# Performance work log

Hardware: AMD Instinct MI355X
Metric: run time of the kernel (lower is better)

The kernel has to match this reference:

```python
import jax, jax.numpy as jnp
import numpy as np

NUM_HEADS = 16


def setup_inputs() -> dict:
    key = jax.random.key(0)
    ks = jax.random.split(key, 6)
    B, N, M, C = 2, 2048, 2048, 1024
    return {
        "reference_data": jax.random.normal(ks[0], (B, N, C), dtype=jnp.float32),
        "target_data": jax.random.normal(ks[1], (B, M, C), dtype=jnp.float32),
        "Wq": jax.random.normal(ks[2], (C, C), dtype=jnp.float32) * (C ** -0.5),
        "Wkv": jax.random.normal(ks[3], (C, 2 * C), dtype=jnp.float32) * (C ** -0.5),
        "Wproj": jax.random.normal(ks[4], (C, C), dtype=jnp.float32) * (C ** -0.5),
        "bproj": jnp.zeros((C,), dtype=jnp.float32),
    }


def reference(reference_data, target_data, Wq, Wkv, Wproj, bproj):
    B, N, C = reference_data.shape
    M = target_data.shape[1]
    H = NUM_HEADS
    hd = C // H
    scale = hd ** -0.5
    # k, v from reference: [B, N, 2, H, hd] -> two [B, H, N, hd]
    kv = (reference_data @ Wkv).reshape(B, N, 2, H, hd)
    k = jnp.transpose(kv[:, :, 0], (0, 2, 1, 3))  # [B,H,N,hd]
    v = jnp.transpose(kv[:, :, 1], (0, 2, 1, 3))  # [B,H,N,hd]
    # q from target: [B, H, M, hd]
    q = jnp.transpose((target_data @ Wq).reshape(B, M, H, hd), (0, 2, 1, 3))
    attn = jnp.einsum("bhid,bhjd->bhij", q, k) * scale  # [B,H,M,N]
    attn = jax.nn.softmax(attn, axis=-1)
    x = jnp.einsum("bhij,bhjd->bhid", attn, v)  # [B,H,M,hd]
    x = jnp.transpose(x, (0, 2, 1, 3)).reshape(B, M, C)
    return x @ Wproj + bproj
```

## Files before the change

kernel.cpp:

```cpp
#include <hip/hip_runtime.h>
#include <hip/hip_bf16.h>
#include <stdint.h>

#define SEQ   2048
#define CH    1024
#define NH    16
#define HD    64

typedef short bf8 __attribute__((ext_vector_type(8)));
typedef short bf4 __attribute__((ext_vector_type(4)));
typedef float f4  __attribute__((ext_vector_type(4)));
typedef unsigned short u16;

#define GAS(p) ((const __attribute__((address_space(1))) void*)(p))
#define LAS(p) ((__attribute__((address_space(3))) void*)(p))

__device__ __forceinline__ u16 f2bf(float f) {
  uint32_t u = __float_as_uint(f);
  u += 0x7fffu + ((u >> 16) & 1u);
  return (u16)(u >> 16);
}

__device__ __forceinline__ uint32_t pk2bf(float a, float b) {
  float2 f; f.x = a; f.y = b;
  __hip_bfloat162 h = __float22bfloat162_rn(f);
  union { __hip_bfloat162 h; uint32_t u; } cv; cv.h = h;
  return cv.u;
}

__device__ __forceinline__ f4 MFMA32(bf8 a, bf8 b, f4 c) {
  return __builtin_amdgcn_mfma_f32_16x16x32_bf16(a, b, c, 0, 0, 0);
}

__device__ __forceinline__ f4 MFMA16(bf4 a, bf4 b, f4 c) {
#if __has_builtin(__builtin_amdgcn_mfma_f32_16x16x16_bf16)
  return __builtin_amdgcn_mfma_f32_16x16x16_bf16(a, b, c, 0, 0, 0);
#elif __has_builtin(__builtin_amdgcn_mfma_f32_16x16x16bf16_1k)
  return __builtin_amdgcn_mfma_f32_16x16x16bf16_1k(a, b, c, 0, 0, 0);
#else
  f4 d = c;
  asm volatile("v_mfma_f32_16x16x16_bf16 %0, %1, %2, %0"
               : "+v"(d) : "v"(a), "v"(b));
  return d;
#endif
}

__global__ void prep(const float* __restrict__ ref, u16* __restrict__ refb,
                     const float* __restrict__ tgt, u16* __restrict__ tgtb,
                     const float* __restrict__ Wq, u16* __restrict__ Wqt,
                     const float* __restrict__ Wkv, u16* __restrict__ Wkvt,
                     const float* __restrict__ Wp, u16* __restrict__ Wpt) {
  __shared__ float tile[32][33];
  int blk = blockIdx.x;
  int t = threadIdx.x;
  if (blk < 8192) {
    const float* in; u16* out;
    if (blk < 4096) { in = ref; out = refb; } else { in = tgt; out = tgtb; blk -= 4096; }
    int i = (blk * 256 + t) * 4;
    float4 f = *reinterpret_cast<const float4*>(in + i);
    ushort4 o;
    o.x = f2bf(f.x); o.y = f2bf(f.y); o.z = f2bf(f.z); o.w = f2bf(f.w);
    *reinterpret_cast<ushort4*>(out + i) = o;
    return;
  }
  blk -= 8192;
  int x = blk & 127, by = blk >> 7;
  const float* in; u16* out; int N;
  if (x < 32)       { in = Wq;  out = Wqt;  N = CH;     }
  else if (x < 96)  { in = Wkv; out = Wkvt; N = 2 * CH; x -= 32; }
  else              { in = Wp;  out = Wpt;  N = CH;     x -= 96; }
  const int K = CH;
  int bn = x * 32, bk = by * 32;
  int tx = t & 31, ty = t >> 5;
  #pragma unroll
  for (int i = ty; i < 32; i += 8)
    tile[i][tx] = in[(size_t)(bk + i) * N + bn + tx];
  __syncthreads();
  #pragma unroll
  for (int i = ty; i < 32; i += 8)
    out[(size_t)(bn + i) * K + bk + tx] = f2bf(tile[tx][i]);
}

__global__ __launch_bounds__(256, 3)
void gemm_qkv(const u16* __restrict__ tgtb, const u16* __restrict__ refb,
              const u16* __restrict__ Wqt, const u16* __restrict__ Wkvt,
              u16* __restrict__ qb, u16* __restrict__ karr, u16* __restrict__ varr)
{
  __shared__ __align__(16) u16 As[2][4096];
  __shared__ __align__(16) u16 Bs[2][4096];
  const int tid = threadIdx.x;
  const int lane = tid & 63, wave = tid >> 6;
  const int l16 = lane & 15, q = lane >> 4;
  const bool isQ = blockIdx.x >= 16;
  const u16* A  = isQ ? tgtb : refb;
  const u16* Bt = isQ ? Wqt : Wkvt;
  const int n0 = (isQ ? (blockIdx.x - 16) : blockIdx.x) * 128;
  const int m0 = blockIdx.y * 128;
  const int wm = (wave >> 1) * 64, wn = (wave & 1) * 64;
  const int Kdim = CH;
  const int c = tid, c2 = tid + 256;
  const int ar = c >> 2, ac = (c & 3) << 3, ar2 = c2 >> 2, ac2 = (c2 & 3) << 3;

  f4 acc[4][4] = {};

  #define STAGE_G(buf, k0)                                                      \
    { __builtin_amdgcn_global_load_lds(                                         \
          GAS(&A[(size_t)(m0 + ar) * Kdim + (k0) + ac]),                        \
          LAS(&As[buf][c << 3]), 16, 0, 0);                                     \
      __builtin_amdgcn_global_load_lds(                                         \
          GAS(&A[(size_t)(m0 + ar2) * Kdim + (k0) + ac2]),                      \
          LAS(&As[buf][c2 << 3]), 16, 0, 0);                                    \
      __builtin_amdgcn_global_load_lds(                                         \
          GAS(&Bt[(size_t)(n0 + ar) * Kdim + (k0) + ac]),                       \
          LAS(&Bs[buf][c << 3]), 16, 0, 0);                                     \
      __builtin_amdgcn_global_load_lds(                                         \
          GAS(&Bt[(size_t)(n0 + ar2) * Kdim + (k0) + ac2]),                     \
          LAS(&Bs[buf][c2 << 3]), 16, 0, 0); }

  STAGE_G(0, 0);
  for (int kk = 0; kk < 32; ++kk) {
    __syncthreads();
    if (kk < 31) STAGE_G((kk + 1) & 1, (kk + 1) * 32);
    const u16* as = As[kk & 1];
    const u16* bs = Bs[kk & 1];
    bf8 a[4], b[4];
    #pragma unroll
    for (int i = 0; i < 4; ++i)
      a[i] = *reinterpret_cast<const bf8*>(&as[(wm + i * 16 + l16) * 32 + q * 8]);
    #pragma unroll
    for (int j = 0; j < 4; ++j)
      b[j] = *reinterpret_cast<const bf8*>(&bs[(wn + j * 16 + l16) * 32 + q * 8]);
    #pragma unroll
    for (int i = 0; i < 4; ++i)
      #pragma unroll
      for (int j = 0; j < 4; ++j)
        acc[i][j] = MFMA32(a[i], b[j], acc[i][j]);
  }
  #undef STAGE_G

  #pragma unroll
  for (int i = 0; i < 4; ++i) {
    const int mbase = m0 + wm + i * 16 + q * 4;
    const int b = mbase >> 11, ns0 = mbase & (SEQ - 1);
    #pragma unroll
    for (int j = 0; j < 4; ++j) {
      const int n = n0 + wn + j * 16 + l16;
      if (isQ) {
        int h = n >> 6, d = n & 63;
        #pragma unroll
        for (int r = 0; r < 4; ++r)
          qb[(size_t)((b * NH + h) * SEQ + ns0 + r) * HD + d] =
              f2bf(acc[i][j][r] * 0.1803368801f);
      } else if (n < CH) {
        int h = n >> 6, d = n & 63;
        size_t base = (size_t)(b * NH + h) * SEQ * HD;
        int off = (((ns0 >> 4) * 2 + (d >> 5)) * 4 + ((d >> 3) & 3)) * 128
                  + (d & 7);
        #pragma unroll
        for (int r = 0; r < 4; ++r)
          karr[base + off + ((ns0 + r) & 15) * 8] = f2bf(acc[i][j][r]);
      } else {
        int c2v = n - CH, h = c2v >> 6, d = c2v & 63;
        size_t base = (size_t)(b * NH + h) * SEQ * HD;
        int off = (((ns0 >> 4) * 2 + (d >> 5)) * 4 + ((ns0 >> 2) & 3)) * 128
                  + (d & 15) * 8 + ((d >> 4) & 1) * 4;
        ushort4 st;
        st.x = f2bf(acc[i][j][0]); st.y = f2bf(acc[i][j][1]);
        st.z = f2bf(acc[i][j][2]); st.w = f2bf(acc[i][j][3]);
        *reinterpret_cast<ushort4*>(&varr[base + off]) = st;
      }
    }
  }
}

__global__ __launch_bounds__(256, 2)
void gemm_proj(const u16* __restrict__ A, const u16* __restrict__ Bt,
               float* __restrict__ fo, const float* __restrict__ bias)
{
  __shared__ __align__(16) u16 As[2][2048];
  __shared__ __align__(16) u16 Bs[2][4096];
  const int tid = threadIdx.x;
  const int lane = tid & 63, wave = tid >> 6;
  const int l16 = lane & 15, q = lane >> 4;
  const int m0 = blockIdx.y * 64, n0 = blockIdx.x * 128;
  const int wm = (wave >> 1) * 32, wn = (wave & 1) * 64;
  const int Kdim = CH;
  const int c = tid, c2 = tid + 256;
  const int ar = c >> 2, ac = (c & 3) << 3, ar2 = c2 >> 2, ac2 = (c2 & 3) << 3;

  f4 acc[2][4] = {};

  #define STAGE_P(buf, k0)                                                      \
    { __builtin_amdgcn_global_load_lds(                                         \
          GAS(&A[(size_t)(m0 + (ar >> 1)) * Kdim + (k0) + ((c & 7) << 2) * 2]), \
          LAS(&As[buf][(c & 255) << 3]), 16, 0, 0);                             \
      __builtin_amdgcn_global_load_lds(                                         \
          GAS(&Bt[(size_t)(n0 + ar) * Kdim + (k0) + ac]),                       \
          LAS(&Bs[buf][c << 3]), 16, 0, 0);                                     \
      __builtin_amdgcn_global_load_lds(                                         \
          GAS(&Bt[(size_t)(n0 + ar2) * Kdim + (k0) + ac2]),                     \
          LAS(&Bs[buf][c2 << 3]), 16, 0, 0); }

  #undef STAGE_P
  const int aar = c >> 2;
  const int aac = (c & 3) << 3;
  #define STAGE_P(buf, k0)                                                      \
    { __builtin_amdgcn_global_load_lds(                                         \
          GAS(&A[(size_t)(m0 + aar) * Kdim + (k0) + aac]),                      \
          LAS(&As[buf][c << 3]), 16, 0, 0);                                     \
      __builtin_amdgcn_global_load_lds(                                         \
          GAS(&Bt[(size_t)(n0 + ar) * Kdim + (k0) + ac]),                       \
          LAS(&Bs[buf][c << 3]), 16, 0, 0);                                     \
      __builtin_amdgcn_global_load_lds(                                         \
          GAS(&Bt[(size_t)(n0 + ar2) * Kdim + (k0) + ac2]),                     \
          LAS(&Bs[buf][c2 << 3]), 16, 0, 0); }

  STAGE_P(0, 0);
  for (int kk = 0; kk < 32; ++kk) {
    __syncthreads();
    if (kk < 31) STAGE_P((kk + 1) & 1, (kk + 1) * 32);
    const u16* as = As[kk & 1];
    const u16* bs = Bs[kk & 1];
    bf8 a[2], b[4];
    #pragma unroll
    for (int i = 0; i < 2; ++i)
      a[i] = *reinterpret_cast<const bf8*>(&as[(wm + i * 16 + l16) * 32 + q * 8]);
    #pragma unroll
    for (int j = 0; j < 4; ++j)
      b[j] = *reinterpret_cast<const bf8*>(&bs[(wn + j * 16 + l16) * 32 + q * 8]);
    #pragma unroll
    for (int i = 0; i < 2; ++i)
      #pragma unroll
      for (int j = 0; j < 4; ++j)
        acc[i][j] = MFMA32(a[i], b[j], acc[i][j]);
  }
  #undef STAGE_P

  #pragma unroll
  for (int i = 0; i < 2; ++i) {
    const int mbase = m0 + wm + i * 16 + q * 4;
    #pragma unroll
    for (int j = 0; j < 4; ++j) {
      const int n = n0 + wn + j * 16 + l16;
      #pragma unroll
      for (int r = 0; r < 4; ++r)
        fo[(size_t)(mbase + r) * CH + n] = acc[i][j][r] + bias[n];
    }
  }
}

__global__ __launch_bounds__(512, 4)
void attn(const u16* __restrict__ Q, const u16* __restrict__ Karr,
          const u16* __restrict__ Varr, u16* __restrict__ X)
{
  __shared__ __align__(16) u16 Ks[2][8192];
  __shared__ __align__(16) u16 Vs[2][8192];
  const int tid = threadIdx.x;
  const int lane = tid & 63;
  const int l16 = lane & 15, q = lane >> 4;
  const int bh = blockIdx.y;
  const int m0 = blockIdx.x * 128;
  const int wm = (tid >> 6) * 16;

  const u16* Qb = Q    + (size_t)bh * SEQ * HD;
  const u16* Kb = Karr + (size_t)bh * SEQ * HD;
  const u16* Vb = Varr + (size_t)bh * SEQ * HD;

  bf8 qf[2];
  #pragma unroll
  for (int ks = 0; ks < 2; ++ks)
    qf[ks] = *reinterpret_cast<const bf8*>(
        &Qb[(size_t)(m0 + wm + l16) * HD + ks * 32 + q * 8]);

  const short one_bf = 0x3F80;
  const bf4 ones = {one_bf, one_bf, one_bf, one_bf};

  f4 o[4] = {};
  f4 ds = {};

  #define STAGE_A(buf, t)                                                       \
    { const u16* kg = Kb + (size_t)(t) * 8192;                                  \
      const u16* vg = Vb + (size_t)(t) * 8192;                                  \
      _Pragma("unroll")                                                         \
      for (int s = 0; s < 2; ++s) {                                             \
        int cc = tid + s * 512;                                                 \
        __builtin_amdgcn_global_load_lds(GAS(kg + cc * 8),                      \
                                         LAS(&Ks[buf][cc * 8]), 16, 0, 0);      \
        __builtin_amdgcn_global_load_lds(GAS(vg + cc * 8),                      \
                                         LAS(&Vs[buf][cc * 8]), 16, 0, 0);      \
      } }

  STAGE_A(0, 0);
  for (int t = 0; t < SEQ / 128; ++t) {
    __syncthreads();
    if (t < SEQ / 128 - 1) STAGE_A((t + 1) & 1, t + 1);
    const u16* ks = Ks[t & 1];
    const u16* vs = Vs[t & 1];

    bf4 pa[8];
    #pragma unroll
    for (int j = 0; j < 8; ++j) {
      bf8 kf0 = *reinterpret_cast<const bf8*>(&ks[((j * 2 + 0) * 4 + q) * 128 + l16 * 8]);
      bf8 kf1 = *reinterpret_cast<const bf8*>(&ks[((j * 2 + 1) * 4 + q) * 128 + l16 * 8]);
      f4 z = {};
      z = MFMA32(kf0, qf[0], z);
      z = MFMA32(kf1, qf[1], z);
      union { bf4 v; uint32_t u[2]; } w;
      w.u[0] = pk2bf(exp2f(z[0]), exp2f(z[1]));
      w.u[1] = pk2bf(exp2f(z[2]), exp2f(z[3]));
      pa[j] = w.v;
    }

    #pragma unroll
    for (int j = 0; j < 8; ++j) {
      ds = MFMA16(pa[j], ones, ds);
      #pragma unroll
      for (int dh = 0; dh < 2; ++dh) {
        bf8 vv = *reinterpret_cast<const bf8*>(&vs[((j * 2 + dh) * 4 + q) * 128 + l16 * 8]);
        bf4 v0 = __builtin_shufflevector(vv, vv, 0, 1, 2, 3);
        bf4 v1 = __builtin_shufflevector(vv, vv, 4, 5, 6, 7);
        o[dh * 2 + 0] = MFMA16(pa[j], v0, o[dh * 2 + 0]);
        o[dh * 2 + 1] = MFMA16(pa[j], v1, o[dh * 2 + 1]);
      }
    }
  }
  #undef STAGE_A

  const int b = bh >> 4, h = bh & (NH - 1);
  #pragma unroll
  for (int r = 0; r < 4; ++r) {
    float ir = 1.0f / ds[r];
    int m = m0 + wm + q * 4 + r;
    #pragma unroll
    for (int dt = 0; dt < 4; ++dt) {
      int d = dt * 16 + l16;
      X[(size_t)(b * SEQ + m) * CH + h * HD + d] = f2bf(o[dt][r] * ir);
    }
  }
}

extern "C" void kernel_launch(void* const* d_in, const int* in_sizes, int n_in,
                              void* d_out, int out_size, void* d_ws, size_t ws_size,
                              hipStream_t stream) {
  const float* ref   = (const float*)d_in[0];
  const float* tgt   = (const float*)d_in[1];
  const float* Wq    = (const float*)d_in[2];
  const float* Wkv   = (const float*)d_in[3];
  const float* Wproj = (const float*)d_in[4];
  const float* bproj = (const float*)d_in[5];
  float* out = (float*)d_out;

  char* ws = (char*)d_ws;
  u16* refb = (u16*)(ws);
  u16* tgtb = (u16*)(ws + (8  << 20));
  u16* Wqt  = (u16*)(ws + (16 << 20));
  u16* Wkvt = (u16*)(ws + (18 << 20));
  u16* Wpt  = (u16*)(ws + (22 << 20));
  u16* qb   = (u16*)(ws + (24 << 20));
  u16* karr = (u16*)(ws + (32 << 20));
  u16* varr = (u16*)(ws + (40 << 20));
  u16* xb   = (u16*)(ws + (48 << 20));

  prep<<<12288, 256, 0, stream>>>(ref, refb, tgt, tgtb, Wq, Wqt, Wkv, Wkvt, Wproj, Wpt);

  gemm_qkv<<<dim3(24, 32), 256, 0, stream>>>(tgtb, refb, Wqt, Wkvt, qb, karr, varr);

  attn<<<dim3(16, 32), 512, 0, stream>>>(qb, karr, varr, xb);

  gemm_proj<<<dim3(8, 64), 256, 0, stream>>>(xb, Wpt, out, bproj);
}
```

Measured before the change: 214.1 us.

## Split attention over key sequence into two partial passes with combine kernel

Splits the attention kernel's key/value loop into two halves along a new grid z dimension. Each half writes an unnormalized numerator (bf16) and a row-sum denominator into buffers reused from dead workspace, and a new combine kernel sums the halves, normalizes, and writes the head-interleaved output. The goal is more blocks for better occupancy; the double-buffered LDS staging is replaced by single-buffered loads with an extra barrier. The GEMM grids are also flattened to 1D with a different block-to-tile order. The extra kernel launch and the round trip through memory add traffic, and storing partial numerators in bf16 adds rounding error.

```diff
diff --git a/kernel.cpp b/kernel.cpp
--- a/kernel.cpp
+++ b/kernel.cpp
@@ -6,6 +6,7 @@
 #define CH    1024
 #define NH    16
 #define HD    64
+#define NUMEL (2 * NH * SEQ * HD)
 
 typedef short bf8 __attribute__((ext_vector_type(8)));
 typedef short bf4 __attribute__((ext_vector_type(4)));
@@ -19,6 +20,10 @@
   uint32_t u = __float_as_uint(f);
   u += 0x7fffu + ((u >> 16) & 1u);
   return (u16)(u >> 16);
+}
+
+__device__ __forceinline__ float bf2f(u16 v) {
+  return __uint_as_float(((uint32_t)v) << 16);
 }
 
 __device__ __forceinline__ uint32_t pk2bf(float a, float b) {
@@ -91,11 +96,13 @@
   const int tid = threadIdx.x;
   const int lane = tid & 63, wave = tid >> 6;
   const int l16 = lane & 15, q = lane >> 4;
-  const bool isQ = blockIdx.x >= 16;
+  const int blk = blockIdx.x;
+  const int n_idx = blk >> 5, m_idx = blk & 31;
+  const bool isQ = n_idx >= 16;
   const u16* A  = isQ ? tgtb : refb;
   const u16* Bt = isQ ? Wqt : Wkvt;
-  const int n0 = (isQ ? (blockIdx.x - 16) : blockIdx.x) * 128;
-  const int m0 = blockIdx.y * 128;
+  const int n0 = (isQ ? (n_idx - 16) : n_idx) * 128;
+  const int m0 = m_idx * 128;
   const int wm = (wave >> 1) * 64, wn = (wave & 1) * 64;
   const int Kdim = CH;
   const int c = tid, c2 = tid + 256;
@@ -182,28 +189,16 @@
   const int tid = threadIdx.x;
   const int lane = tid & 63, wave = tid >> 6;
   const int l16 = lane & 15, q = lane >> 4;
-  const int m0 = blockIdx.y * 64, n0 = blockIdx.x * 128;
+  const int blk = blockIdx.x;
+  const int m0 = (blk & 63) * 64, n0 = (blk >> 6) * 128;
   const int wm = (wave >> 1) * 32, wn = (wave & 1) * 64;
   const int Kdim = CH;
   const int c = tid, c2 = tid + 256;
   const int ar = c >> 2, ac = (c & 3) << 3, ar2 = c2 >> 2, ac2 = (c2 & 3) << 3;
+  const int aar = c >> 2, aac = (c & 3) << 3;
 
   f4 acc[2][4] = {};
 
-  #define STAGE_P(buf, k0)                                                      \
-    { __builtin_amdgcn_global_load_lds(                                         \
-          GAS(&A[(size_t)(m0 + (ar >> 1)) * Kdim + (k0) + ((c & 7) << 2) * 2]), \
-          LAS(&As[buf][(c & 255) << 3]), 16, 0, 0);                             \
-      __builtin_amdgcn_global_load_lds(                                         \
-          GAS(&Bt[(size_t)(n0 + ar) * Kdim + (k0) + ac]),                       \
-          LAS(&Bs[buf][c << 3]), 16, 0, 0);                                     \
-      __builtin_amdgcn_global_load_lds(                                         \
-          GAS(&Bt[(size_t)(n0 + ar2) * Kdim + (k0) + ac2]),                     \
-          LAS(&Bs[buf][c2 << 3]), 16, 0, 0); }
-
-  #undef STAGE_P
-  const int aar = c >> 2;
-  const int aac = (c & 3) << 3;
   #define STAGE_P(buf, k0)                                                      \
     { __builtin_amdgcn_global_load_lds(                                         \
           GAS(&A[(size_t)(m0 + aar) * Kdim + (k0) + aac]),                      \
@@ -249,17 +244,19 @@
   }
 }
 
-__global__ __launch_bounds__(512, 4)
+__global__ __launch_bounds__(512, 8)
 void attn(const u16* __restrict__ Q, const u16* __restrict__ Karr,
-          const u16* __restrict__ Varr, u16* __restrict__ X)
+          const u16* __restrict__ Varr, u16* __restrict__ num,
+          float* __restrict__ den)
 {
-  __shared__ __align__(16) u16 Ks[2][8192];
-  __shared__ __align__(16) u16 Vs[2][8192];
+  __shared__ __align__(16) u16 Ks[8192];
+  __shared__ __align__(16) u16 Vs[8192];
   const int tid = threadIdx.x;
   const int lane = tid & 63;
   const int l16 = lane & 15, q = lane >> 4;
   const int bh = blockIdx.y;
   const int m0 = blockIdx.x * 128;
+  const int sp = blockIdx.z;
   const int wm = (tid >> 6) * 16;
 
   const u16* Qb = Q    + (size_t)bh * SEQ * HD;
@@ -278,30 +275,27 @@
   f4 o[4] = {};
   f4 ds = {};
 
-  #define STAGE_A(buf, t)                                                       \
-    { const u16* kg = Kb + (size_t)(t) * 8192;                                  \
-      const u16* vg = Vb + (size_t)(t) * 8192;                                  \
-      _Pragma("unroll")                                                         \
-      for (int s = 0; s < 2; ++s) {                                             \
-        int cc = tid + s * 512;                                                 \
-        __builtin_amdgcn_global_load_lds(GAS(kg + cc * 8),                      \
-                                         LAS(&Ks[buf][cc * 8]), 16, 0, 0);      \
-        __builtin_amdgcn_global_load_lds(GAS(vg + cc * 8),                      \
-                                         LAS(&Vs[buf][cc * 8]), 16, 0, 0);      \
-      } }
-
-  STAGE_A(0, 0);
-  for (int t = 0; t < SEQ / 128; ++t) {
+  const int t0 = sp * 8;
+  for (int t = 0; t < 8; ++t) {
+    const int tt = t0 + t;
     __syncthreads();
-    if (t < SEQ / 128 - 1) STAGE_A((t + 1) & 1, t + 1);
-    const u16* ks = Ks[t & 1];
-    const u16* vs = Vs[t & 1];
+    {
+      const u16* kg = Kb + (size_t)tt * 8192;
+      const u16* vg = Vb + (size_t)tt * 8192;
+      #pragma unroll
+      for (int s = 0; s < 2; ++s) {
+        int cc = tid + s * 512;
+        __builtin_amdgcn_global_load_lds(GAS(kg + cc * 8), LAS(&Ks[cc * 8]), 16, 0, 0);
+        __builtin_amdgcn_global_load_lds(GAS(vg + cc * 8), LAS(&Vs[cc * 8]), 16, 0, 0);
+      }
+    }
+    __syncthreads();
 
     bf4 pa[8];
     #pragma unroll
     for (int j = 0; j < 8; ++j) {
-      bf8 kf0 = *reinterpret_cast<const bf8*>(&ks[((j * 2 + 0) * 4 + q) * 128 + l16 * 8]);
-      bf8 kf1 = *reinterpret_cast<const bf8*>(&ks[((j * 2 + 1) * 4 + q) * 128 + l16 * 8]);
+      bf8 kf0 = *reinterpret_cast<const bf8*>(&Ks[((j * 2 + 0) * 4 + q) * 128 + l16 * 8]);
+      bf8 kf1 = *reinterpret_cast<const bf8*>(&Ks[((j * 2 + 1) * 4 + q) * 128 + l16 * 8]);
       f4 z = {};
       z = MFMA32(kf0, qf[0], z);
       z = MFMA32(kf1, qf[1], z);
@@ -316,7 +310,7 @@
       ds = MFMA16(pa[j], ones, ds);
       #pragma unroll
       for (int dh = 0; dh < 2; ++dh) {
-        bf8 vv = *reinterpret_cast<const bf8*>(&vs[((j * 2 + dh) * 4 + q) * 128 + l16 * 8]);
+        bf8 vv = *reinterpret_cast<const bf8*>(&Vs[((j * 2 + dh) * 4 + q) * 128 + l16 * 8]);
         bf4 v0 = __builtin_shufflevector(vv, vv, 0, 1, 2, 3);
         bf4 v1 = __builtin_shufflevector(vv, vv, 4, 5, 6, 7);
         o[dh * 2 + 0] = MFMA16(pa[j], v0, o[dh * 2 + 0]);
@@ -324,19 +318,36 @@
       }
     }
   }
-  #undef STAGE_A
-
-  const int b = bh >> 4, h = bh & (NH - 1);
+
+  u16* nh = num + (size_t)sp * NUMEL;
+  float* dh_ = den + (size_t)sp * (2 * NH * SEQ);
   #pragma unroll
   for (int r = 0; r < 4; ++r) {
-    float ir = 1.0f / ds[r];
     int m = m0 + wm + q * 4 + r;
-    #pragma unroll
-    for (int dt = 0; dt < 4; ++dt) {
-      int d = dt * 16 + l16;
-      X[(size_t)(b * SEQ + m) * CH + h * HD + d] = f2bf(o[dt][r] * ir);
-    }
-  }
+    if (l16 == 0) dh_[bh * SEQ + m] = ds[r];
+    #pragma unroll
+    for (int dt = 0; dt < 4; ++dt)
+      nh[((size_t)bh * SEQ + m) * HD + dt * 16 + l16] = f2bf(o[dt][r]);
+  }
+}
+
+__global__ void combine(const u16* __restrict__ num, const float* __restrict__ den,
+                        u16* __restrict__ xb) {
+  int idx = (blockIdx.x * 256 + threadIdx.x) * 4;
+  int bh = idx >> 17;
+  int rem = idx & (SEQ * HD - 1);
+  int m = rem >> 6, d = rem & 63;
+  ushort4 a = *reinterpret_cast<const ushort4*>(num + idx);
+  ushort4 b4 = *reinterpret_cast<const ushort4*>(num + NUMEL + idx);
+  float dsum = den[bh * SEQ + m] + den[2 * NH * SEQ + bh * SEQ + m];
+  float inv = 1.0f / dsum;
+  int b = bh >> 4, h = bh & (NH - 1);
+  ushort4 o;
+  o.x = f2bf((bf2f(a.x) + bf2f(b4.x)) * inv);
+  o.y = f2bf((bf2f(a.y) + bf2f(b4.y)) * inv);
+  o.z = f2bf((bf2f(a.z) + bf2f(b4.z)) * inv);
+  o.w = f2bf((bf2f(a.w) + bf2f(b4.w)) * inv);
+  *reinterpret_cast<ushort4*>(&xb[(size_t)(b * SEQ + m) * CH + h * HD + d]) = o;
 }
 
 extern "C" void kernel_launch(void* const* d_in, const int* in_sizes, int n_in,
@@ -360,12 +371,16 @@
   u16* karr = (u16*)(ws + (32 << 20));
   u16* varr = (u16*)(ws + (40 << 20));
   u16* xb   = (u16*)(ws + (48 << 20));
+  u16* nbuf  = refb;
+  float* dbuf = (float*)Wqt;
 
   prep<<<12288, 256, 0, stream>>>(ref, refb, tgt, tgtb, Wq, Wqt, Wkv, Wkvt, Wproj, Wpt);
 
-  gemm_qkv<<<dim3(24, 32), 256, 0, stream>>>(tgtb, refb, Wqt, Wkvt, qb, karr, varr);
-
-  attn<<<dim3(16, 32), 512, 0, stream>>>(qb, karr, varr, xb);
-
-  gemm_proj<<<dim3(8, 64), 256, 0, stream>>>(xb, Wpt, out, bproj);
-}
+  gemm_qkv<<<768, 256, 0, stream>>>(tgtb, refb, Wqt, Wkvt, qb, karr, varr);
+
+  attn<<<dim3(16, 32, 2), 512, 0, stream>>>(qb, karr, varr, nbuf, dbuf);
+
+  combine<<<4096, 256, 0, stream>>>(nbuf, dbuf, xb);
+
+  gemm_proj<<<512, 256, 0, stream>>>(xb, Wpt, out, bproj);
+}
```

Result: no change. 217.2 us (+1.5%).
